# Optimization experiments

Measured on AMD Instinct MI355X. Metric: run time of the kernel, lower is better.

Reference implementation:

```python
import jax, jax.numpy as jnp
import numpy as np

N_DETS = 16384
DEG = 32
E = N_DETS * DEG
NUM_BLOCKS = 4
SHORTCUT = 128   # shortcutDim
RED = 32         # reducedDim
INNER = 64       # blockInnerDim = 2*32
PW_IN = 9        # pwfeatRawInput
PW_HID = 256     # pwfeatInnerDim
PW_OUT = 32      # pwfeatOutDim


def _xavier(key, shape):
    fan_in, fan_out = shape[-2], shape[-1]
    lim = jnp.sqrt(6.0 / (fan_in + fan_out)).astype(jnp.float32)
    return jax.random.uniform(key, shape, jnp.float32, -lim, lim)


def setup_inputs() -> dict:
    key = jax.random.key(0)
    ks = jax.random.split(key, 24)
    inp = {}
    inp["detFeatures"] = jnp.zeros((N_DETS, SHORTCUT), jnp.float32)
    inp["pairRaw"] = jax.random.normal(ks[0], (E, PW_IN), jnp.float32)
    # every detection has DEG neighbor rows (sorted, all segments non-empty)
    inp["cIdxs"] = jnp.repeat(jnp.arange(N_DETS, dtype=jnp.int32), DEG)
    inp["nIdxs"] = jax.random.randint(ks[1], (E,), 0, N_DETS, jnp.int32)
    # pairwise-feature generator MLP: 9 -> 256 -> 256 -> 32
    inp["g_W1"] = _xavier(ks[2], (PW_IN, PW_HID)); inp["g_b1"] = jnp.zeros((PW_HID,), jnp.float32)
    inp["g_W2"] = _xavier(ks[3], (PW_HID, PW_HID)); inp["g_b2"] = jnp.zeros((PW_HID,), jnp.float32)
    inp["g_W3"] = _xavier(ks[4], (PW_HID, PW_OUT)); inp["g_b3"] = jnp.zeros((PW_OUT,), jnp.float32)
    # per-block params, stacked along leading block dim
    inp["blk_fc1_W"] = _xavier(ks[5], (NUM_BLOCKS, SHORTCUT, RED)); inp["blk_fc1_b"] = jnp.zeros((NUM_BLOCKS, RED), jnp.float32)
    inp["blk_pw_W1"] = _xavier(ks[6], (NUM_BLOCKS, 3 * RED, INNER)); inp["blk_pw_b1"] = jnp.zeros((NUM_BLOCKS, INNER), jnp.float32)
    inp["blk_pw_W2"] = _xavier(ks[7], (NUM_BLOCKS, INNER, INNER)); inp["blk_pw_b2"] = jnp.zeros((NUM_BLOCKS, INNER), jnp.float32)
    inp["blk_post_W1"] = _xavier(ks[8], (NUM_BLOCKS, INNER, INNER)); inp["blk_post_b1"] = jnp.zeros((NUM_BLOCKS, INNER), jnp.float32)
    inp["blk_post_W2"] = _xavier(ks[9], (NUM_BLOCKS, INNER, INNER)); inp["blk_post_b2"] = jnp.zeros((NUM_BLOCKS, INNER), jnp.float32)
    inp["blk_out_W"] = _xavier(ks[10], (NUM_BLOCKS, INNER, SHORTCUT)); inp["blk_out_b"] = jnp.zeros((NUM_BLOCKS, SHORTCUT), jnp.float32)
    inp["s_W"] = _xavier(ks[11], (3, SHORTCUT, SHORTCUT)); inp["s_b"] = jnp.zeros((3, SHORTCUT), jnp.float32)
    inp["pred_W"] = _xavier(ks[12], (SHORTCUT, 1)); inp["pred_b"] = jnp.zeros((1,), jnp.float32)
    return inp


def reference(detFeatures, pairRaw, cIdxs, nIdxs,
              g_W1, g_b1, g_W2, g_b2, g_W3, g_b3,
              blk_fc1_W, blk_fc1_b, blk_pw_W1, blk_pw_b1, blk_pw_W2, blk_pw_b2,
              blk_post_W1, blk_post_b1, blk_post_W2, blk_post_b2,
              blk_out_W, blk_out_b, s_W, s_b, pred_W, pred_b):
    relu = jax.nn.relu
    n_dets = detFeatures.shape[0]
    num_blocks = blk_fc1_W.shape[0]
    # GNet.pairwiseFeaturesFC: pwfeat generator MLP on raw 9-d pair descriptors
    pair = relu(pairRaw @ g_W1 + g_b1)          # (E, 256)
    pair = relu(pair @ g_W2 + g_b2)             # (E, 256)
    pair = relu(pair @ g_W3 + g_b3)             # (E, 32)
    is_id = (cIdxs == nIdxs)[:, None]           # zero-out self-neighbor feats
    x = detFeatures                             # (N, 128)
    for b in range(num_blocks):                 # structurally distinct blocks
        f = relu(x @ blk_fc1_W[b] + blk_fc1_b[b])          # (N, 32)
        cF = f[cIdxs]                                       # (E, 32) gather
        nF = jnp.where(is_id, jnp.float32(0), f[nIdxs])     # (E, 32) gather
        h = jnp.concatenate([pair, cF, nF], axis=1)         # (E, 96)
        h = relu(h @ blk_pw_W1[b] + blk_pw_b1[b])           # (E, 64)
        h = relu(h @ blk_pw_W2[b] + blk_pw_b2[b])           # (E, 64)
        # per-detection max pooling over neighbor rows (segment-max)
        m = jax.ops.segment_max(h, cIdxs, num_segments=n_dets,
                                indices_are_sorted=True)    # (N, 64)
        m = relu(m @ blk_post_W1[b] + blk_post_b1[b])
        m = relu(m @ blk_post_W2[b] + blk_post_b2[b])
        x = relu(x + m @ blk_out_W[b] + blk_out_b[b])        # residual + relu
    for i in range(s_W.shape[0]):
        x = relu(x @ s_W[i] + s_b[i])
    scores = (x @ pred_W + pred_b).reshape(-1)               # (N,)
    return scores
```

## Files before the change

kernel.cpp:

```cpp
#include <hip/hip_runtime.h>

#define N_DETS 16384
#define DEG 32
#define E_EDGES (N_DETS * DEG)
#define PAIR_GRID 512

typedef __attribute__((ext_vector_type(8))) short bf16x8;
typedef __attribute__((ext_vector_type(4))) float f32x4;

__device__ __forceinline__ ushort f32_to_bf16(float v) {
  unsigned u = __float_as_uint(v);
  u += 0x7FFFu + ((u >> 16) & 1u);
  return (ushort)(u >> 16);
}
__device__ __forceinline__ float bf16_to_f32(ushort h) {
  return __uint_as_float((unsigned)h << 16);
}

__global__ __launch_bounds__(256) void split_w_kernel(
    const float* __restrict__ W, ushort* __restrict__ hi, ushort* __restrict__ lo, int N)
{
  const int n = blockIdx.x, k = threadIdx.x;
  const float v = W[(size_t)k * N + n];
  const ushort h = f32_to_bf16(v);
  const ushort l = f32_to_bf16(v - bf16_to_f32(h));
  hi[(size_t)n * 256 + k] = h;
  lo[(size_t)n * 256 + k] = l;
}

__global__ __launch_bounds__(256) void split_edge_w_kernel(
    const float* __restrict__ W1all, const float* __restrict__ W2all,
    ushort* __restrict__ w1h, ushort* __restrict__ w1l,
    ushort* __restrict__ w2h, ushort* __restrict__ w2l)
{
  const int b = blockIdx.x;
  const float* W1 = W1all + b * 6144;
  const float* W2 = W2all + b * 4096;
  for (int i = threadIdx.x; i < 6144; i += 256) {
    const int col = i / 96, k = i % 96;
    const float v = W1[k * 64 + col];
    const ushort h = f32_to_bf16(v);
    w1h[b * 6144 + col * 96 + k] = h;
    w1l[b * 6144 + col * 96 + k] = f32_to_bf16(v - bf16_to_f32(h));
  }
  for (int i = threadIdx.x; i < 4096; i += 256) {
    const int col = i >> 6, k = i & 63;
    const float v = W2[k * 64 + col];
    const ushort h = f32_to_bf16(v);
    w2h[b * 4096 + col * 64 + k] = h;
    w2l[b * 4096 + col * 64 + k] = f32_to_bf16(v - bf16_to_f32(h));
  }
}

#define A_STRIDE 264

__global__ __launch_bounds__(512, 2) void pair_mlp_kernel(
    const float* __restrict__ raw,
    const float* __restrict__ W1, const float* __restrict__ b1,
    const ushort* __restrict__ w2h, const ushort* __restrict__ w2l,
    const float* __restrict__ b2,
    const ushort* __restrict__ w3h, const ushort* __restrict__ w3l,
    const float* __restrict__ b3,
    ushort* __restrict__ pair_h, ushort* __restrict__ pair_l)
{
  __shared__ __align__(16) ushort ah[64 * A_STRIDE];
  __shared__ __align__(16) ushort al[64 * A_STRIDE];
  __shared__ __align__(16) ushort w3sh[32 * A_STRIDE];
  __shared__ __align__(16) ushort w3sl[32 * A_STRIDE];
  __shared__ float rawt[64 * 12];

  const int t = threadIdx.x;
  const int lane = t & 63, wv = t >> 6;
  const int ln = lane & 15, kg = lane >> 4;

  for (int i = t; i < 32 * 64; i += 512) {
    const int row = (i * 4) >> 8, col = (i * 4) & 255;
    *(ushort4*)&w3sh[row * A_STRIDE + col] = *(const ushort4*)&w3h[row * 256 + col];
    *(ushort4*)&w3sl[row * A_STRIDE + col] = *(const ushort4*)&w3l[row * 256 + col];
  }

  bf16x8 b2hreg[2][8], b2lreg[2][8];
  #pragma unroll
  for (int nt = 0; nt < 2; ++nt)
    #pragma unroll
    for (int ks = 0; ks < 8; ++ks) {
      const size_t bo = (size_t)(wv * 32 + nt * 16 + ln) * 256 + ks * 32 + kg * 8;
      b2hreg[nt][ks] = *(const bf16x8*)&w2h[bo];
      b2lreg[nt][ks] = *(const bf16x8*)&w2l[bo];
    }
  float bias2[2];
  #pragma unroll
  for (int nt = 0; nt < 2; ++nt) bias2[nt] = b2[wv * 32 + nt * 16 + ln];
  const int mt3 = wv >> 1, nt3 = wv & 1;
  const float b3v = b3[nt3 * 16 + ln];
  __syncthreads();

  for (int grp = blockIdx.x; grp < E_EDGES / 64; grp += gridDim.x) {
    const long long e0 = (long long)grp * 64;

    for (int i = t; i < 64 * 9; i += 512)
      rawt[(i / 9) * 12 + (i % 9)] = raw[e0 * 9 + i];
    __syncthreads();

    {
      const int col = t & 255, r0 = (t >> 8) * 32;
      float a1[32];
      const float bv = b1[col];
      #pragma unroll
      for (int r = 0; r < 32; ++r) a1[r] = bv;
      #pragma unroll
      for (int k = 0; k < 9; ++k) {
        const float w = W1[k * 256 + col];
        #pragma unroll
        for (int r = 0; r < 32; ++r) a1[r] = fmaf(rawt[(r0 + r) * 12 + k], w, a1[r]);
      }
      #pragma unroll
      for (int r = 0; r < 32; ++r) {
        const float v = fmaxf(a1[r], 0.f);
        const ushort h = f32_to_bf16(v);
        ah[(r0 + r) * A_STRIDE + col] = h;
        al[(r0 + r) * A_STRIDE + col] = f32_to_bf16(v - bf16_to_f32(h));
      }
    }
    __syncthreads();

    f32x4 acc[2][4];
    #pragma unroll
    for (int nt = 0; nt < 2; ++nt)
      #pragma unroll
      for (int mt = 0; mt < 4; ++mt) {
        acc[nt][mt][0] = 0.f; acc[nt][mt][1] = 0.f;
        acc[nt][mt][2] = 0.f; acc[nt][mt][3] = 0.f;
      }
    #pragma unroll
    for (int ks = 0; ks < 8; ++ks) {
      const int ka = ks * 32 + kg * 8;
      bf16x8 ahf[4], alf[4];
      #pragma unroll
      for (int mt = 0; mt < 4; ++mt) {
        ahf[mt] = *(const bf16x8*)&ah[(mt * 16 + ln) * A_STRIDE + ka];
        alf[mt] = *(const bf16x8*)&al[(mt * 16 + ln) * A_STRIDE + ka];
      }
      #pragma unroll
      for (int nt = 0; nt < 2; ++nt)
        #pragma unroll
        for (int mt = 0; mt < 4; ++mt) {
          acc[nt][mt] = __builtin_amdgcn_mfma_f32_16x16x32_bf16(ahf[mt], b2hreg[nt][ks], acc[nt][mt], 0, 0, 0);
          acc[nt][mt] = __builtin_amdgcn_mfma_f32_16x16x32_bf16(alf[mt], b2hreg[nt][ks], acc[nt][mt], 0, 0, 0);
          acc[nt][mt] = __builtin_amdgcn_mfma_f32_16x16x32_bf16(ahf[mt], b2lreg[nt][ks], acc[nt][mt], 0, 0, 0);
        }
    }
    __syncthreads();

    #pragma unroll
    for (int nt = 0; nt < 2; ++nt) {
      const int colg = wv * 32 + nt * 16 + ln;
      #pragma unroll
      for (int mt = 0; mt < 4; ++mt)
        #pragma unroll
        for (int r = 0; r < 4; ++r) {
          const int rowe = mt * 16 + kg * 4 + r;
          const float v = fmaxf(acc[nt][mt][r] + bias2[nt], 0.f);
          const ushort h = f32_to_bf16(v);
          ah[rowe * A_STRIDE + colg] = h;
          al[rowe * A_STRIDE + colg] = f32_to_bf16(v - bf16_to_f32(h));
        }
    }
    __syncthreads();

    f32x4 acc3;
    acc3[0] = 0.f; acc3[1] = 0.f; acc3[2] = 0.f; acc3[3] = 0.f;
    #pragma unroll
    for (int ks = 0; ks < 8; ++ks) {
      const int ka = ks * 32 + kg * 8;
      const bf16x8 a_h = *(const bf16x8*)&ah[(mt3 * 16 + ln) * A_STRIDE + ka];
      const bf16x8 a_l = *(const bf16x8*)&al[(mt3 * 16 + ln) * A_STRIDE + ka];
      const bf16x8 b_h = *(const bf16x8*)&w3sh[(nt3 * 16 + ln) * A_STRIDE + ka];
      const bf16x8 b_l = *(const bf16x8*)&w3sl[(nt3 * 16 + ln) * A_STRIDE + ka];
      acc3 = __builtin_amdgcn_mfma_f32_16x16x32_bf16(a_h, b_h, acc3, 0, 0, 0);
      acc3 = __builtin_amdgcn_mfma_f32_16x16x32_bf16(a_l, b_h, acc3, 0, 0, 0);
      acc3 = __builtin_amdgcn_mfma_f32_16x16x32_bf16(a_h, b_l, acc3, 0, 0, 0);
    }
    const int col3 = nt3 * 16 + ln;
    #pragma unroll
    for (int r = 0; r < 4; ++r) {
      const int rowe = mt3 * 16 + kg * 4 + r;
      const float v = fmaxf(acc3[r] + b3v, 0.f);
      const ushort h = f32_to_bf16(v);
      const size_t idx = (size_t)(e0 + rowe) * 32 + col3;
      pair_h[idx] = h;
      pair_l[idx] = f32_to_bf16(v - bf16_to_f32(h));
    }
    __syncthreads();
  }
}

__global__ __launch_bounds__(256) void fc1_kernel(
    const float* __restrict__ x, const float* __restrict__ W,
    const float* __restrict__ b, float* __restrict__ f,
    ushort* __restrict__ f_h, ushort* __restrict__ f_l)
{
  __shared__ float Wl[128 * 32];
  const int t = threadIdx.x;
  #pragma unroll
  for (int j = 0; j < 4; ++j) {
    const int off = t * 4 + j * 1024;
    *(float4*)&Wl[off] = *(const float4*)&W[off];
  }
  __syncthreads();
  const int c = t & 31, rr = t >> 5;
  const long long r = (long long)blockIdx.x * 8 + rr;
  const float* xr = x + r * 128;
  float acc = b[c];
  #pragma unroll 8
  for (int k = 0; k < 128; k += 4) {
    const float4 a = *(const float4*)&xr[k];
    acc = fmaf(a.x, Wl[(k + 0) * 32 + c], acc);
    acc = fmaf(a.y, Wl[(k + 1) * 32 + c], acc);
    acc = fmaf(a.z, Wl[(k + 2) * 32 + c], acc);
    acc = fmaf(a.w, Wl[(k + 3) * 32 + c], acc);
  }
  const float v = fmaxf(acc, 0.f);
  f[r * 32 + c] = v;
  const ushort h = f32_to_bf16(v);
  f_h[r * 32 + c] = h;
  f_l[r * 32 + c] = f32_to_bf16(v - bf16_to_f32(h));
}

#define W1S 104
#define W2S 72
#define CTS 36

__global__ __launch_bounds__(512, 2) void edge_kernel(
    const ushort* __restrict__ pair_h, const ushort* __restrict__ pair_l,
    const float* __restrict__ f,
    const ushort* __restrict__ f_h, const ushort* __restrict__ f_l,
    const int* __restrict__ nIdxs,
    const float* __restrict__ W1g, const float* __restrict__ bb1,
    const ushort* __restrict__ gw1h, const ushort* __restrict__ gw1l,
    const ushort* __restrict__ gw2h, const ushort* __restrict__ gw2l,
    const float* __restrict__ bb2,
    float* __restrict__ m)
{
  __shared__ __align__(16) ushort W1hS[64 * W1S], W1lS[64 * W1S];
  __shared__ __align__(16) ushort W2hS[64 * W2S], W2lS[64 * W2S];
  __shared__ __align__(16) float  W1cT[64 * CTS];
  __shared__ __align__(16) ushort h1h[8][32 * W2S], h1l[8][32 * W2S];

  const int t = threadIdx.x;
  const int lane = t & 63, wv = t >> 6;
  const int ln = lane & 15, kg = lane >> 4;
  const int d = blockIdx.x * 8 + wv;
  const long long e0 = (long long)d * 32;

  for (int i = t; i < 1536; i += 512) {
    const int idx = i * 4, row = idx / 96, k = idx % 96;
    *(ushort4*)&W1hS[row * W1S + k] = *(const ushort4*)&gw1h[idx];
    *(ushort4*)&W1lS[row * W1S + k] = *(const ushort4*)&gw1l[idx];
  }
  for (int i = t; i < 1024; i += 512) {
    const int idx = i * 4, row = idx >> 6, k = idx & 63;
    *(ushort4*)&W2hS[row * W2S + k] = *(const ushort4*)&gw2h[idx];
    *(ushort4*)&W2lS[row * W2S + k] = *(const ushort4*)&gw2l[idx];
  }
  for (int i = t; i < 2048; i += 512) {
    const int col = i >> 5, j = i & 31;
    W1cT[col * CTS + j] = W1g[(32 + j) * 64 + col];
  }
  __syncthreads();

  float cfs[4];
  {
    const float4 fv0 = *(const float4*)&f[(size_t)d * 32 + kg * 8];
    const float4 fv1 = *(const float4*)&f[(size_t)d * 32 + kg * 8 + 4];
    #pragma unroll
    for (int nt = 0; nt < 4; ++nt) {
      const int col = nt * 16 + ln;
      const float4 w0 = *(const float4*)&W1cT[col * CTS + kg * 8];
      const float4 w1 = *(const float4*)&W1cT[col * CTS + kg * 8 + 4];
      float s = fv0.x * w0.x + fv0.y * w0.y + fv0.z * w0.z + fv0.w * w0.w
              + fv1.x * w1.x + fv1.y * w1.y + fv1.z * w1.z + fv1.w * w1.w;
      s += __shfl_xor(s, 16);
      s += __shfl_xor(s, 32);
      cfs[nt] = s + bb1[col];
    }
  }

  f32x4 acc1[4][2];
  #pragma unroll
  for (int nt = 0; nt < 4; ++nt)
    #pragma unroll
    for (int mt = 0; mt < 2; ++mt) {
      acc1[nt][mt][0] = 0.f; acc1[nt][mt][1] = 0.f;
      acc1[nt][mt][2] = 0.f; acc1[nt][mt][3] = 0.f;
    }
  bf16x8 ph[2], pl_[2], nh[2], nl_[2];
  #pragma unroll
  for (int mt = 0; mt < 2; ++mt) {
    const long long row = e0 + mt * 16 + ln;
    ph[mt]  = *(const bf16x8*)&pair_h[row * 32 + kg * 8];
    pl_[mt] = *(const bf16x8*)&pair_l[row * 32 + kg * 8];
    const int n = nIdxs[row];
    bf16x8 vh = *(const bf16x8*)&f_h[(size_t)n * 32 + kg * 8];
    bf16x8 vl = *(const bf16x8*)&f_l[(size_t)n * 32 + kg * 8];
    if (n == d) { vh = (bf16x8){0,0,0,0,0,0,0,0}; vl = (bf16x8){0,0,0,0,0,0,0,0}; }
    nh[mt] = vh; nl_[mt] = vl;
  }
  #pragma unroll
  for (int nt = 0; nt < 4; ++nt) {
    const int bro = (nt * 16 + ln) * W1S;
    const bf16x8 b0h = *(const bf16x8*)&W1hS[bro + kg * 8];
    const bf16x8 b0l = *(const bf16x8*)&W1lS[bro + kg * 8];
    const bf16x8 b1h = *(const bf16x8*)&W1hS[bro + 64 + kg * 8];
    const bf16x8 b1l = *(const bf16x8*)&W1lS[bro + 64 + kg * 8];
    #pragma unroll
    for (int mt = 0; mt < 2; ++mt) {
      acc1[nt][mt] = __builtin_amdgcn_mfma_f32_16x16x32_bf16(ph[mt], b0h, acc1[nt][mt], 0, 0, 0);
      acc1[nt][mt] = __builtin_amdgcn_mfma_f32_16x16x32_bf16(pl_[mt], b0h, acc1[nt][mt], 0, 0, 0);
      acc1[nt][mt] = __builtin_amdgcn_mfma_f32_16x16x32_bf16(ph[mt], b0l, acc1[nt][mt], 0, 0, 0);
      acc1[nt][mt] = __builtin_amdgcn_mfma_f32_16x16x32_bf16(nh[mt], b1h, acc1[nt][mt], 0, 0, 0);
      acc1[nt][mt] = __builtin_amdgcn_mfma_f32_16x16x32_bf16(nl_[mt], b1h, acc1[nt][mt], 0, 0, 0);
      acc1[nt][mt] = __builtin_amdgcn_mfma_f32_16x16x32_bf16(nh[mt], b1l, acc1[nt][mt], 0, 0, 0);
    }
  }

  #pragma unroll
  for (int nt = 0; nt < 4; ++nt) {
    const int col = nt * 16 + ln;
    #pragma unroll
    for (int mt = 0; mt < 2; ++mt)
      #pragma unroll
      for (int r = 0; r < 4; ++r) {
        const int row = mt * 16 + kg * 4 + r;
        const float v = fmaxf(acc1[nt][mt][r] + cfs[nt], 0.f);
        const ushort h = f32_to_bf16(v);
        h1h[wv][row * W2S + col] = h;
        h1l[wv][row * W2S + col] = f32_to_bf16(v - bf16_to_f32(h));
      }
  }

  f32x4 acc2[4][2];
  #pragma unroll
  for (int mt = 0; mt < 4; ++mt)
    #pragma unroll
    for (int nt = 0; nt < 2; ++nt) {
      acc2[mt][nt][0] = 0.f; acc2[mt][nt][1] = 0.f;
      acc2[mt][nt][2] = 0.f; acc2[mt][nt][3] = 0.f;
    }
  #pragma unroll
  for (int ks = 0; ks < 2; ++ks) {
    const int ka = ks * 32 + kg * 8;
    bf16x8 bh[2], bl[2];
    #pragma unroll
    for (int nt = 0; nt < 2; ++nt) {
      bh[nt] = *(const bf16x8*)&h1h[wv][(nt * 16 + ln) * W2S + ka];
      bl[nt] = *(const bf16x8*)&h1l[wv][(nt * 16 + ln) * W2S + ka];
    }
    #pragma unroll
    for (int mt = 0; mt < 4; ++mt) {
      const bf16x8 a_h = *(const bf16x8*)&W2hS[(mt * 16 + ln) * W2S + ka];
      const bf16x8 a_l = *(const bf16x8*)&W2lS[(mt * 16 + ln) * W2S + ka];
      #pragma unroll
      for (int nt = 0; nt < 2; ++nt) {
        acc2[mt][nt] = __builtin_amdgcn_mfma_f32_16x16x32_bf16(a_h, bh[nt], acc2[mt][nt], 0, 0, 0);
        acc2[mt][nt] = __builtin_amdgcn_mfma_f32_16x16x32_bf16(a_h, bl[nt], acc2[mt][nt], 0, 0, 0);
        acc2[mt][nt] = __builtin_amdgcn_mfma_f32_16x16x32_bf16(a_l, bh[nt], acc2[mt][nt], 0, 0, 0);
      }
    }
  }

  #pragma unroll
  for (int mt = 0; mt < 4; ++mt)
    #pragma unroll
    for (int r = 0; r < 4; ++r) {
      float mx = fmaxf(acc2[mt][0][r], acc2[mt][1][r]);
      mx = fmaxf(mx, __shfl_xor(mx, 1));
      mx = fmaxf(mx, __shfl_xor(mx, 2));
      mx = fmaxf(mx, __shfl_xor(mx, 4));
      mx = fmaxf(mx, __shfl_xor(mx, 8));
      if (ln == mt * 4 + r) {
        const int outcol = mt * 16 + kg * 4 + r;
        m[(size_t)d * 64 + outcol] = fmaxf(mx + bb2[outcol], 0.f);
      }
    }
}

__global__ __launch_bounds__(256) void post12_kernel(
    const float* __restrict__ m,
    const float* __restrict__ W1, const float* __restrict__ b1,
    const float* __restrict__ W2, const float* __restrict__ b2,
    float* __restrict__ mm)
{
  __shared__ float Wl[64 * 64];
  __shared__ float mt[32 * 64];
  __shared__ float ht[32 * 64];
  const int t = threadIdx.x;
  const int c = t & 63, g = t >> 6;
  const long long r0 = (long long)blockIdx.x * 32;
  #pragma unroll
  for (int j = 0; j < 4; ++j) {
    const int off = t * 4 + j * 1024;
    *(float4*)&Wl[off] = *(const float4*)&W1[off];
  }
  #pragma unroll
  for (int j = 0; j < 2; ++j) {
    const int off = t * 4 + j * 1024;
    *(float4*)&mt[off] = *(const float4*)&m[r0 * 64 + off];
  }
  __syncthreads();
  float acc[8];
  {
    const float bv = b1[c];
    #pragma unroll
    for (int i = 0; i < 8; ++i) acc[i] = bv;
  }
  #pragma unroll 4
  for (int k = 0; k < 64; k += 4) {
    const float w0 = Wl[(k + 0) * 64 + c], w1 = Wl[(k + 1) * 64 + c];
    const float w2 = Wl[(k + 2) * 64 + c], w3 = Wl[(k + 3) * 64 + c];
    #pragma unroll
    for (int i = 0; i < 8; ++i) {
      const float4 a = *(const float4*)&mt[(g * 8 + i) * 64 + k];
      acc[i] = fmaf(a.x, w0, fmaf(a.y, w1, fmaf(a.z, w2, fmaf(a.w, w3, acc[i]))));
    }
  }
  #pragma unroll
  for (int i = 0; i < 8; ++i) ht[(g * 8 + i) * 64 + c] = fmaxf(acc[i], 0.f);
  __syncthreads();
  #pragma unroll
  for (int j = 0; j < 4; ++j) {
    const int off = t * 4 + j * 1024;
    *(float4*)&Wl[off] = *(const float4*)&W2[off];
  }
  __syncthreads();
  float acc2[8];
  {
    const float bv = b2[c];
    #pragma unroll
    for (int i = 0; i < 8; ++i) acc2[i] = bv;
  }
  #pragma unroll 4
  for (int k = 0; k < 64; k += 4) {
    const float w0 = Wl[(k + 0) * 64 + c], w1 = Wl[(k + 1) * 64 + c];
    const float w2 = Wl[(k + 2) * 64 + c], w3 = Wl[(k + 3) * 64 + c];
    #pragma unroll
    for (int i = 0; i < 8; ++i) {
      const float4 a = *(const float4*)&ht[(g * 8 + i) * 64 + k];
      acc2[i] = fmaf(a.x, w0, fmaf(a.y, w1, fmaf(a.z, w2, fmaf(a.w, w3, acc2[i]))));
    }
  }
  #pragma unroll
  for (int i = 0; i < 8; ++i)
    mm[(r0 + g * 8 + i) * 64 + c] = fmaxf(acc2[i], 0.f);
}

__global__ __launch_bounds__(256) void postout_kernel(
    const float* __restrict__ x, const float* __restrict__ mmv,
    const float* __restrict__ W, const float* __restrict__ bias,
    float* __restrict__ y)
{
  __shared__ float Wl[64 * 128];
  __shared__ float mt[16 * 64];
  const int t = threadIdx.x;
  const int c = t & 127, g = t >> 7;
  const long long r0 = (long long)blockIdx.x * 16;
  #pragma unroll
  for (int j = 0; j < 8; ++j) {
    const int off = t * 4 + j * 1024;
    *(float4*)&Wl[off] = *(const float4*)&W[off];
  }
  {
    const int off = t * 4;
    *(float4*)&mt[off] = *(const float4*)&mmv[r0 * 64 + off];
  }
  __syncthreads();
  float acc[8];
  {
    const float bv = bias[c];
    #pragma unroll
    for (int i = 0; i < 8; ++i) acc[i] = bv;
  }
  #pragma unroll 4
  for (int k = 0; k < 64; k += 4) {
    const float w0 = Wl[(k + 0) * 128 + c], w1 = Wl[(k + 1) * 128 + c];
    const float w2 = Wl[(k + 2) * 128 + c], w3 = Wl[(k + 3) * 128 + c];
    #pragma unroll
    for (int i = 0; i < 8; ++i) {
      const float4 a = *(const float4*)&mt[(g * 8 + i) * 64 + k];
      acc[i] = fmaf(a.x, w0, fmaf(a.y, w1, fmaf(a.z, w2, fmaf(a.w, w3, acc[i]))));
    }
  }
  #pragma unroll
  for (int i = 0; i < 8; ++i) {
    const long long idx = (r0 + g * 8 + i) * 128 + c;
    y[idx] = fmaxf(x[idx] + acc[i], 0.f);
  }
}

__global__ __launch_bounds__(256) void score_layer_kernel(
    const float* __restrict__ x, const float* __restrict__ W,
    const float* __restrict__ bias, float* __restrict__ y)
{
  __shared__ float Wl[64 * 128];
  __shared__ float xt[16 * 128];
  const int t = threadIdx.x;
  const int c = t & 127, g = t >> 7;
  const long long r0 = (long long)blockIdx.x * 16;
  #pragma unroll
  for (int j = 0; j < 2; ++j) {
    const int off = t * 4 + j * 1024;
    *(float4*)&xt[off] = *(const float4*)&x[r0 * 128 + off];
  }
  float acc[8];
  {
    const float bv = bias[c];
    #pragma unroll
    for (int i = 0; i < 8; ++i) acc[i] = bv;
  }
  #pragma unroll 1
  for (int kc = 0; kc < 128; kc += 64) {
    __syncthreads();
    #pragma unroll
    for (int j = 0; j < 8; ++j) {
      const int off = t * 4 + j * 1024;
      *(float4*)&Wl[off] = *(const float4*)&W[(long long)kc * 128 + off];
    }
    __syncthreads();
    #pragma unroll 4
    for (int k = 0; k < 64; k += 4) {
      const float w0 = Wl[(k + 0) * 128 + c], w1 = Wl[(k + 1) * 128 + c];
      const float w2 = Wl[(k + 2) * 128 + c], w3 = Wl[(k + 3) * 128 + c];
      #pragma unroll
      for (int i = 0; i < 8; ++i) {
        const float4 a = *(const float4*)&xt[(g * 8 + i) * 128 + kc + k];
        acc[i] = fmaf(a.x, w0, fmaf(a.y, w1, fmaf(a.z, w2, fmaf(a.w, w3, acc[i]))));
      }
    }
  }
  #pragma unroll
  for (int i = 0; i < 8; ++i)
    y[(r0 + g * 8 + i) * 128 + c] = fmaxf(acc[i], 0.f);
}

__global__ __launch_bounds__(256) void dot_kernel(
    const float* __restrict__ x, const float* __restrict__ pW,
    const float* __restrict__ pb, float* __restrict__ out)
{
  const int t = threadIdx.x;
  const int l = t & 63;
  const long long r = (long long)blockIdx.x * 4 + (t >> 6);
  const float* xr = x + r * 128;
  float acc = fmaf(xr[l], pW[l], xr[l + 64] * pW[l + 64]);
  for (int o = 32; o; o >>= 1) acc += __shfl_xor(acc, o);
  if (l == 0) out[r] = acc + pb[0];
}

extern "C" void kernel_launch(void* const* d_in, const int* in_sizes, int n_in,
                              void* d_out, int out_size, void* d_ws, size_t ws_size,
                              hipStream_t stream)
{
  const float* detF    = (const float*)d_in[0];
  const float* pairRaw = (const float*)d_in[1];
  const int*   cIdx    = (const int*)d_in[2];
  const int*   nIdx    = (const int*)d_in[3];
  const float* gW1 = (const float*)d_in[4];   const float* gb1 = (const float*)d_in[5];
  const float* gW2 = (const float*)d_in[6];   const float* gb2 = (const float*)d_in[7];
  const float* gW3 = (const float*)d_in[8];   const float* gb3 = (const float*)d_in[9];
  const float* fc1W = (const float*)d_in[10]; const float* fc1b = (const float*)d_in[11];
  const float* pwW1 = (const float*)d_in[12]; const float* pwb1 = (const float*)d_in[13];
  const float* pwW2 = (const float*)d_in[14]; const float* pwb2 = (const float*)d_in[15];
  const float* poW1 = (const float*)d_in[16]; const float* pob1 = (const float*)d_in[17];
  const float* poW2 = (const float*)d_in[18]; const float* pob2 = (const float*)d_in[19];
  const float* outW = (const float*)d_in[20]; const float* outb = (const float*)d_in[21];
  const float* sW = (const float*)d_in[22];   const float* sb = (const float*)d_in[23];
  const float* predW = (const float*)d_in[24]; const float* predb = (const float*)d_in[25];
  float* out = (float*)d_out;
  (void)cIdx;

  ushort* w2h  = (ushort*)d_ws;
  ushort* w2l  = w2h + 65536;
  ushort* w3h  = w2l + 65536;
  ushort* w3l  = w3h + 8192;
  ushort* w1eh = w3l + 8192;
  ushort* w1el = w1eh + 24576;
  ushort* w2eh = w1el + 24576;
  ushort* w2el = w2eh + 16384;
  ushort* pair_h = w2el + 16384;
  ushort* pair_l = pair_h + (size_t)E_EDGES * 32;
  ushort* f_h    = pair_l + (size_t)E_EDGES * 32;
  ushort* f_l    = f_h + (size_t)N_DETS * 32;
  float* f  = (float*)(f_l + (size_t)N_DETS * 32);
  float* m  = f  + (size_t)N_DETS * 32;
  float* mm = m  + (size_t)N_DETS * 64;
  float* xa = mm + (size_t)N_DETS * 64;
  float* xb = xa + (size_t)N_DETS * 128;

  hipMemcpyAsync(xa, detF, (size_t)N_DETS * 128 * sizeof(float),
                 hipMemcpyDeviceToDevice, stream);

  split_w_kernel<<<256, 256, 0, stream>>>(gW2, w2h, w2l, 256);
  split_w_kernel<<<32, 256, 0, stream>>>(gW3, w3h, w3l, 32);
  split_edge_w_kernel<<<4, 256, 0, stream>>>(pwW1, pwW2, w1eh, w1el, w2eh, w2el);

  pair_mlp_kernel<<<PAIR_GRID, 512, 0, stream>>>(pairRaw, gW1, gb1,
      w2h, w2l, gb2, w3h, w3l, gb3, pair_h, pair_l);

  float* xin = xa;
  float* xout = xb;
  for (int b = 0; b < 4; ++b) {
    fc1_kernel<<<N_DETS / 8, 256, 0, stream>>>(xin, fc1W + b * 4096, fc1b + b * 32,
        f, f_h, f_l);
    edge_kernel<<<N_DETS / 8, 512, 0, stream>>>(pair_h, pair_l, f, f_h, f_l, nIdx,
        pwW1 + b * 6144, pwb1 + b * 64,
        w1eh + b * 6144, w1el + b * 6144, w2eh + b * 4096, w2el + b * 4096,
        pwb2 + b * 64, m);
    post12_kernel<<<N_DETS / 32, 256, 0, stream>>>(m, poW1 + b * 4096, pob1 + b * 64,
        poW2 + b * 4096, pob2 + b * 64, mm);
    postout_kernel<<<N_DETS / 16, 256, 0, stream>>>(xin, mm, outW + b * 8192, outb + b * 128, xout);
    float* tmp = xout; xout = xin; xin = tmp;
  }
  for (int i = 0; i < 3; ++i) {
    score_layer_kernel<<<N_DETS / 16, 256, 0, stream>>>(xin, sW + i * 16384, sb + i * 128, xout);
    float* tmp = xout; xout = xin; xin = tmp;
  }
  dot_kernel<<<N_DETS / 4, 256, 0, stream>>>(xin, predW, predb, out);
}
```

Baseline: 839.7 us.

## Fuse post MLP with output projection and slim pair MLP shared memory

Merges the post12 and postout kernels into one, so the 64-wide intermediate stays in shared memory and one launch per block disappears. In the pair MLP, the W3 shared-memory staging is removed and W3 fragments are read straight from global memory. This cuts LDS use enough to raise the occupancy hint from 2 to 4 blocks. The first-layer loop is also reordered to keep the 9 weights in registers and read each raw row with vector loads. The risks are extra global traffic for W3, register spills under the tighter launch bound, and a larger LDS footprint (about 65 KB) in the fused post kernel.

```diff
diff --git a/kernel.cpp b/kernel.cpp
--- a/kernel.cpp
+++ b/kernel.cpp
@@ -54,7 +54,7 @@
 
 #define A_STRIDE 264
 
-__global__ __launch_bounds__(512, 2) void pair_mlp_kernel(
+__global__ __launch_bounds__(512, 4) void pair_mlp_kernel(
     const float* __restrict__ raw,
     const float* __restrict__ W1, const float* __restrict__ b1,
     const ushort* __restrict__ w2h, const ushort* __restrict__ w2l,
@@ -65,19 +65,11 @@
 {
   __shared__ __align__(16) ushort ah[64 * A_STRIDE];
   __shared__ __align__(16) ushort al[64 * A_STRIDE];
-  __shared__ __align__(16) ushort w3sh[32 * A_STRIDE];
-  __shared__ __align__(16) ushort w3sl[32 * A_STRIDE];
-  __shared__ float rawt[64 * 12];
+  __shared__ __align__(16) float rawt[64 * 12];
 
   const int t = threadIdx.x;
   const int lane = t & 63, wv = t >> 6;
   const int ln = lane & 15, kg = lane >> 4;
-
-  for (int i = t; i < 32 * 64; i += 512) {
-    const int row = (i * 4) >> 8, col = (i * 4) & 255;
-    *(ushort4*)&w3sh[row * A_STRIDE + col] = *(const ushort4*)&w3h[row * 256 + col];
-    *(ushort4*)&w3sl[row * A_STRIDE + col] = *(const ushort4*)&w3l[row * 256 + col];
-  }
 
   bf16x8 b2hreg[2][8], b2lreg[2][8];
   #pragma unroll
@@ -93,7 +85,8 @@
   for (int nt = 0; nt < 2; ++nt) bias2[nt] = b2[wv * 32 + nt * 16 + ln];
   const int mt3 = wv >> 1, nt3 = wv & 1;
   const float b3v = b3[nt3 * 16 + ln];
-  __syncthreads();
+  const ushort* w3hp = w3h + (size_t)(nt3 * 16 + ln) * 256;
+  const ushort* w3lp = w3l + (size_t)(nt3 * 16 + ln) * 256;
 
   for (int grp = blockIdx.x; grp < E_EDGES / 64; grp += gridDim.x) {
     const long long e0 = (long long)grp * 64;
@@ -104,19 +97,22 @@
 
     {
       const int col = t & 255, r0 = (t >> 8) * 32;
-      float a1[32];
       const float bv = b1[col];
-      #pragma unroll
-      for (int r = 0; r < 32; ++r) a1[r] = bv;
-      #pragma unroll
-      for (int k = 0; k < 9; ++k) {
-        const float w = W1[k * 256 + col];
-        #pragma unroll
-        for (int r = 0; r < 32; ++r) a1[r] = fmaf(rawt[(r0 + r) * 12 + k], w, a1[r]);
-      }
+      float wk[9];
+      #pragma unroll
+      for (int k = 0; k < 9; ++k) wk[k] = W1[k * 256 + col];
       #pragma unroll
       for (int r = 0; r < 32; ++r) {
-        const float v = fmaxf(a1[r], 0.f);
+        const float4 ra = *(const float4*)&rawt[(r0 + r) * 12];
+        const float4 rb = *(const float4*)&rawt[(r0 + r) * 12 + 4];
+        const float rc = rawt[(r0 + r) * 12 + 8];
+        float s = bv;
+        s = fmaf(ra.x, wk[0], s); s = fmaf(ra.y, wk[1], s);
+        s = fmaf(ra.z, wk[2], s); s = fmaf(ra.w, wk[3], s);
+        s = fmaf(rb.x, wk[4], s); s = fmaf(rb.y, wk[5], s);
+        s = fmaf(rb.z, wk[6], s); s = fmaf(rb.w, wk[7], s);
+        s = fmaf(rc, wk[8], s);
+        const float v = fmaxf(s, 0.f);
         const ushort h = f32_to_bf16(v);
         ah[(r0 + r) * A_STRIDE + col] = h;
         al[(r0 + r) * A_STRIDE + col] = f32_to_bf16(v - bf16_to_f32(h));
@@ -175,8 +171,8 @@
       const int ka = ks * 32 + kg * 8;
       const bf16x8 a_h = *(const bf16x8*)&ah[(mt3 * 16 + ln) * A_STRIDE + ka];
       const bf16x8 a_l = *(const bf16x8*)&al[(mt3 * 16 + ln) * A_STRIDE + ka];
-      const bf16x8 b_h = *(const bf16x8*)&w3sh[(nt3 * 16 + ln) * A_STRIDE + ka];
-      const bf16x8 b_l = *(const bf16x8*)&w3sl[(nt3 * 16 + ln) * A_STRIDE + ka];
+      const bf16x8 b_h = *(const bf16x8*)&w3hp[ka];
+      const bf16x8 b_l = *(const bf16x8*)&w3lp[ka];
       acc3 = __builtin_amdgcn_mfma_f32_16x16x32_bf16(a_h, b_h, acc3, 0, 0, 0);
       acc3 = __builtin_amdgcn_mfma_f32_16x16x32_bf16(a_l, b_h, acc3, 0, 0, 0);
       acc3 = __builtin_amdgcn_mfma_f32_16x16x32_bf16(a_h, b_l, acc3, 0, 0, 0);
@@ -385,13 +381,15 @@
     }
 }
 
-__global__ __launch_bounds__(256) void post12_kernel(
-    const float* __restrict__ m,
+__global__ __launch_bounds__(256) void post_fused_kernel(
+    const float* __restrict__ m, const float* __restrict__ x,
     const float* __restrict__ W1, const float* __restrict__ b1,
     const float* __restrict__ W2, const float* __restrict__ b2,
-    float* __restrict__ mm)
+    const float* __restrict__ Wo, const float* __restrict__ bo,
+    float* __restrict__ y)
 {
   __shared__ float Wl[64 * 64];
+  __shared__ float Wlo[64 * 128];
   __shared__ float mt[32 * 64];
   __shared__ float ht[32 * 64];
   const int t = threadIdx.x;
@@ -403,6 +401,11 @@
     *(float4*)&Wl[off] = *(const float4*)&W1[off];
   }
   #pragma unroll
+  for (int j = 0; j < 8; ++j) {
+    const int off = t * 4 + j * 1024;
+    *(float4*)&Wlo[off] = *(const float4*)&Wo[off];
+  }
+  #pragma unroll
   for (int j = 0; j < 2; ++j) {
     const int off = t * 4 + j * 1024;
     *(float4*)&mt[off] = *(const float4*)&m[r0 * 64 + off];
@@ -450,50 +453,29 @@
     }
   }
   #pragma unroll
-  for (int i = 0; i < 8; ++i)
-    mm[(r0 + g * 8 + i) * 64 + c] = fmaxf(acc2[i], 0.f);
-}
-
-__global__ __launch_bounds__(256) void postout_kernel(
-    const float* __restrict__ x, const float* __restrict__ mmv,
-    const float* __restrict__ W, const float* __restrict__ bias,
-    float* __restrict__ y)
-{
-  __shared__ float Wl[64 * 128];
-  __shared__ float mt[16 * 64];
-  const int t = threadIdx.x;
-  const int c = t & 127, g = t >> 7;
-  const long long r0 = (long long)blockIdx.x * 16;
-  #pragma unroll
-  for (int j = 0; j < 8; ++j) {
-    const int off = t * 4 + j * 1024;
-    *(float4*)&Wl[off] = *(const float4*)&W[off];
-  }
+  for (int i = 0; i < 8; ++i) mt[(g * 8 + i) * 64 + c] = fmaxf(acc2[i], 0.f);
+  __syncthreads();
+  const int c2 = t & 127, g2 = t >> 7;
+  float acco[16];
   {
-    const int off = t * 4;
-    *(float4*)&mt[off] = *(const float4*)&mmv[r0 * 64 + off];
-  }
-  __syncthreads();
-  float acc[8];
-  {
-    const float bv = bias[c];
-    #pragma unroll
-    for (int i = 0; i < 8; ++i) acc[i] = bv;
+    const float bv = bo[c2];
+    #pragma unroll
+    for (int i = 0; i < 16; ++i) acco[i] = bv;
   }
   #pragma unroll 4
   for (int k = 0; k < 64; k += 4) {
-    const float w0 = Wl[(k + 0) * 128 + c], w1 = Wl[(k + 1) * 128 + c];
-    const float w2 = Wl[(k + 2) * 128 + c], w3 = Wl[(k + 3) * 128 + c];
-    #pragma unroll
-    for (int i = 0; i < 8; ++i) {
-      const float4 a = *(const float4*)&mt[(g * 8 + i) * 64 + k];
-      acc[i] = fmaf(a.x, w0, fmaf(a.y, w1, fmaf(a.z, w2, fmaf(a.w, w3, acc[i]))));
-    }
-  }
-  #pragma unroll
-  for (int i = 0; i < 8; ++i) {
-    const long long idx = (r0 + g * 8 + i) * 128 + c;
-    y[idx] = fmaxf(x[idx] + acc[i], 0.f);
+    const float w0 = Wlo[(k + 0) * 128 + c2], w1 = Wlo[(k + 1) * 128 + c2];
+    const float w2 = Wlo[(k + 2) * 128 + c2], w3 = Wlo[(k + 3) * 128 + c2];
+    #pragma unroll
+    for (int i = 0; i < 16; ++i) {
+      const float4 a = *(const float4*)&mt[(g2 * 16 + i) * 64 + k];
+      acco[i] = fmaf(a.x, w0, fmaf(a.y, w1, fmaf(a.z, w2, fmaf(a.w, w3, acco[i]))));
+    }
+  }
+  #pragma unroll
+  for (int i = 0; i < 16; ++i) {
+    const long long idx = (r0 + g2 * 16 + i) * 128 + c2;
+    y[idx] = fmaxf(x[idx] + acco[i], 0.f);
   }
 }
 
@@ -614,9 +596,9 @@
         pwW1 + b * 6144, pwb1 + b * 64,
         w1eh + b * 6144, w1el + b * 6144, w2eh + b * 4096, w2el + b * 4096,
         pwb2 + b * 64, m);
-    post12_kernel<<<N_DETS / 32, 256, 0, stream>>>(m, poW1 + b * 4096, pob1 + b * 64,
-        poW2 + b * 4096, pob2 + b * 64, mm);
-    postout_kernel<<<N_DETS / 16, 256, 0, stream>>>(xin, mm, outW + b * 8192, outb + b * 128, xout);
+    post_fused_kernel<<<N_DETS / 32, 256, 0, stream>>>(m, xin,
+        poW1 + b * 4096, pob1 + b * 64, poW2 + b * 4096, pob2 + b * 64,
+        outW + b * 8192, outb + b * 128, xout);
     float* tmp = xout; xout = xin; xin = tmp;
   }
   for (int i = 0; i < 3; ++i) {
```

After: 1.043 ms. 1.24x slower.
